# Kernel tuning notes

Measured on AMD Instinct MI355X. Metric: run time of the kernel, lower is better.

The kernel has to match this reference:

```python
import jax, jax.numpy as jnp
import numpy as np

EPS = 1e-12  # torch F.normalize eps

def _l2norm(t):
    # normalize over last axis (tokens N), matching F.normalize(dim=-1)
    n = jnp.sqrt(jnp.sum(t * t, axis=-1, keepdims=True))
    return t / jnp.maximum(n, EPS)

def setup_inputs() -> dict:
    key = jax.random.key(0)
    ks = jax.random.split(key, 4)
    B, N, C, H = 16, 3136, 768, 16
    x = jax.random.normal(ks[0], (B, N, C), dtype=jnp.float32)
    w_qkv = jax.random.normal(ks[1], (3 * C, C), dtype=jnp.float32) * (C ** -0.5)
    temperature = jnp.ones((H, 1, 1), dtype=jnp.float32)
    w_proj = jax.random.normal(ks[2], (C, C), dtype=jnp.float32) * (C ** -0.5)
    b_proj = jnp.zeros((C,), dtype=jnp.float32)
    return {"x": x, "w_qkv": w_qkv, "temperature": temperature,
            "w_proj": w_proj, "b_proj": b_proj}

def reference(x, w_qkv, temperature, w_proj, b_proj):
    B, N, C = x.shape
    H = temperature.shape[0]
    dh = C // H
    # qkv: [B,N,3C] -> [B,N,3,H,dh] -> [3,B,H,dh,N]
    qkv = (x @ w_qkv.T).reshape(B, N, 3, H, dh)
    qkv = jnp.transpose(qkv, (2, 0, 3, 4, 1))
    q, k, v = qkv[0], qkv[1], qkv[2]          # each [B,H,dh,N]
    q = _l2norm(q)
    k = _l2norm(k)
    # cross-covariance attention over channel axis: [B,H,dh,dh]
    attn = jnp.einsum('bhdn,bhen->bhde', q, k) * temperature
    attn = jax.nn.softmax(attn, axis=-1)
    out = jnp.einsum('bhde,bhen->bhdn', attn, v)  # [B,H,dh,N]
    out = jnp.transpose(out, (0, 3, 1, 2)).reshape(B, N, C)
    return out @ w_proj.T + b_proj
```

## Files before the change

kernel.cpp:

```cpp
#include <hip/hip_runtime.h>
#include <hip/hip_bf16.h>
#include <stdint.h>

using f32x4   = __attribute__((ext_vector_type(4))) float;
using half8   = __attribute__((ext_vector_type(8))) _Float16;
using half4   = __attribute__((ext_vector_type(4))) _Float16;
using float4v = __attribute__((ext_vector_type(4))) float;

typedef const __attribute__((address_space(1))) void gas_void;
typedef __attribute__((address_space(3))) void las_void;

__device__ __forceinline__ void gload_lds16(const void* gptr, void* lptr) {
  __builtin_amdgcn_global_load_lds((gas_void*)(uintptr_t)gptr,
                                   (las_void*)(uintptr_t)lptr, 16, 0, 0);
}

#define MFMA_F16(a, b, c) __builtin_amdgcn_mfma_f32_16x16x32_f16((a), (b), (c), 0, 0, 0)

__global__ void k_cvtw(const float* __restrict__ wqkv, const float* __restrict__ wproj,
                       _Float16* __restrict__ w16, _Float16* __restrict__ wp16,
                       _Float16* __restrict__ wvT) {
  const long N1 = 221184L, N2 = 73728L, N3 = 98304L;
  const long total = N1 + N2 + N3;
  for (long i = (long)blockIdx.x * blockDim.x + threadIdx.x; i < total;
       i += (long)gridDim.x * blockDim.x) {
    if (i < N1 + N2) {
      const float* src; _Float16* dst; long off;
      if (i < N1) { src = wqkv;  dst = w16;  off = i; }
      else        { src = wproj; dst = wp16; off = i - N1; }
      const float4v* p = (const float4v*)(src + off * 8);
      float4v a = p[0], b = p[1];
      half8 o;
      o[0] = (_Float16)a[0]; o[1] = (_Float16)a[1]; o[2] = (_Float16)a[2]; o[3] = (_Float16)a[3];
      o[4] = (_Float16)b[0]; o[5] = (_Float16)b[1]; o[6] = (_Float16)b[2]; o[7] = (_Float16)b[3];
      *(half8*)(dst + off * 8) = o;
    } else {
      const long u = i - N1 - N2;
      const int h = (int)(u / 6144);
      const int r = (int)(u % 6144);
      const int f = r >> 3, e0 = (r & 7) * 8;
      half8 o;
      if (e0 >= 48) {
#pragma unroll
        for (int j = 0; j < 8; ++j) o[j] = (_Float16)0.f;
      } else {
#pragma unroll
        for (int j = 0; j < 8; ++j)
          o[j] = (_Float16)wqkv[(long)(1536 + h * 48 + e0 + j) * 768 + f];
      }
      *(half8*)(wvT + ((long)(h * 768 + f) * 64 + e0)) = o;
    }
  }
}

__global__ __launch_bounds__(256)
void k_cvtx(const float* __restrict__ x, _Float16* __restrict__ x16,
            _Float16* __restrict__ xT) {
  __shared__ _Float16 lt[64 * 68];
  const int bid = blockIdx.x;
  const int b = bid / 588;
  const int rem = bid % 588;
  const int tt = rem / 12, ct = rem % 12;
  const long t0g = (long)b * 3136 + tt * 64;
  const int c0 = ct * 64;
  const int tid = threadIdx.x;
#pragma unroll
  for (int ch = 0; ch < 4; ++ch) {
    const int idx = tid + ch * 256;
    const int tr = idx >> 4, cg = (idx & 15) * 4;
    float4v v = *(const float4v*)&x[(t0g + tr) * 768 + c0 + cg];
    half4 hv;
    hv[0] = (_Float16)v[0]; hv[1] = (_Float16)v[1];
    hv[2] = (_Float16)v[2]; hv[3] = (_Float16)v[3];
    *(half4*)&x16[(t0g + tr) * 768 + c0 + cg] = hv;
    *(half4*)&lt[tr * 68 + cg] = hv;
  }
  __syncthreads();
  const int c = tid >> 2, tch = tid & 3;
  half8 o0, o1;
#pragma unroll
  for (int j = 0; j < 8; ++j) o0[j] = lt[(tch * 16 + j) * 68 + c];
#pragma unroll
  for (int j = 0; j < 8; ++j) o1[j] = lt[(tch * 16 + 8 + j) * 68 + c];
  _Float16* dst = xT + (long)b * 2408448 + (long)(c0 + c) * 3136 + tt * 64 + tch * 16;
  *(half8*)dst = o0;
  *(half8*)(dst + 8) = o1;
}

__global__ __launch_bounds__(256)
void k_gram(const _Float16* __restrict__ xT, _Float16* __restrict__ G) {
  __shared__ _Float16 lds[2][2][128 * 32];
  const int tid = threadIdx.x;
  const int wv = tid >> 6, lane = tid & 63;
  const int g = lane >> 4, cidx = lane & 15;
  const int wr = wv >> 1, wc = wv & 1;

  const int nwg = (int)gridDim.x;
  const int q = nwg >> 3, r = nwg & 7;
  const int xcd = (int)blockIdx.x & 7, bidx = (int)blockIdx.x >> 3;
  int wg = (xcd < r ? xcd * (q + 1) : r * (q + 1) + (xcd - r) * q) + bidx;
  const int b = wg / 21;
  int p = wg % 21;
  int mt = 0;
  while (p >= 6 - mt) { p -= 6 - mt; ++mt; }
  const int nt = mt + p;

  const _Float16* Ab = xT + (long)b * 2408448 + (long)mt * 128 * 3136;
  const _Float16* Bb = xT + (long)b * 2408448 + (long)nt * 128 * 3136;

  const int srow = lane >> 2;
  const int sgr  = (lane & 3) ^ ((lane >> 3) & 3);

  auto stage = [&](int buf, int kt) {
#pragma unroll
    for (int l = 0; l < 2; ++l) {
      const int rbase = wv * 32 + l * 16;
      const long koff = (long)kt * 32 + sgr * 8;
      gload_lds16(Ab + (long)(rbase + srow) * 3136 + koff, &lds[buf][0][rbase * 32]);
      gload_lds16(Bb + (long)(rbase + srow) * 3136 + koff, &lds[buf][1][rbase * 32]);
    }
  };
  const int gr = (g ^ ((cidx >> 1) & 3)) * 8;

  f32x4 acc[4][4] = {};
  stage(0, 0);
  __syncthreads();
  for (int kt = 0; kt < 98; ++kt) {
    const int cur = kt & 1;
    if (kt + 1 < 98) stage(cur ^ 1, kt + 1);
    half8 af[4], bf[4];
#pragma unroll
    for (int m = 0; m < 4; ++m)
      af[m] = *(const half8*)&lds[cur][0][(wr * 64 + m * 16 + cidx) * 32 + gr];
#pragma unroll
    for (int n = 0; n < 4; ++n)
      bf[n] = *(const half8*)&lds[cur][1][(wc * 64 + n * 16 + cidx) * 32 + gr];
#pragma unroll
    for (int m = 0; m < 4; ++m)
#pragma unroll
      for (int n = 0; n < 4; ++n)
        acc[m][n] = MFMA_F16(af[m], bf[n], acc[m][n]);
    __syncthreads();
  }
  _Float16* Gb = G + (long)b * 589824;
  const long m0 = (long)mt * 128, n0 = (long)nt * 128;
#pragma unroll
  for (int m = 0; m < 4; ++m)
#pragma unroll
    for (int rr = 0; rr < 4; ++rr) {
      const long row = m0 + wr * 64 + m * 16 + g * 4 + rr;
#pragma unroll
      for (int n = 0; n < 4; ++n)
        Gb[row * 768 + n0 + wc * 64 + n * 16 + cidx] = (_Float16)acc[m][n][rr];
    }
  if (mt != nt) {
#pragma unroll
    for (int m = 0; m < 4; ++m)
#pragma unroll
      for (int n = 0; n < 4; ++n) {
        half4 hv;
#pragma unroll
        for (int rr = 0; rr < 4; ++rr) hv[rr] = (_Float16)acc[m][n][rr];
        const long col  = n0 + wc * 64 + n * 16 + cidx;
        const long row0 = m0 + wr * 64 + m * 16 + g * 4;
        *(half4*)&Gb[col * 768 + row0] = hv;
      }
  }
}

template<bool OUT_F32>
__global__ __launch_bounds__(256)
void k_g128(const _Float16* __restrict__ A, const _Float16* __restrict__ B,
            void* __restrict__ Cv, const float* __restrict__ bias,
            int Mt, int Nt, long Areal, long Astr, long Bstr, long Cstr,
            long N, long K)
{
  __shared__ _Float16 lds[2][2][128 * 32];
  const int tid = threadIdx.x;
  const int wv = tid >> 6, lane = tid & 63;
  const int g = lane >> 4, cidx = lane & 15;
  const int wr = wv >> 1, wc = wv & 1;

  const int nwg = (int)gridDim.x;
  const int q = nwg >> 3, r = nwg & 7;
  const int xcd = (int)blockIdx.x & 7, bidx = (int)blockIdx.x >> 3;
  int wg = (xcd < r ? xcd * (q + 1) : r * (q + 1) + (xcd - r) * q) + bidx;
  const int tpb = Mt * Nt;
  const int b = wg / tpb;
  const int rem = wg % tpb;
  const int mt = rem % Mt, nt = rem / Mt;
  const long m0 = (long)mt * 128, n0 = (long)nt * 128;

  const _Float16* Ab = A + b * Astr + m0 * K;
  const _Float16* Bb = B + b * Bstr + n0 * K;
  const int nkt = (int)(K >> 5);

  const int srow = lane >> 2;
  const int sgr  = (lane & 3) ^ ((lane >> 3) & 3);

  auto stage = [&](int buf, int kt) {
#pragma unroll
    for (int l = 0; l < 2; ++l) {
      const int rbase = wv * 32 + l * 16;
      const long koff = (long)kt * 32 + sgr * 8;
      gload_lds16(Ab + (long)(rbase + srow) * K + koff, &lds[buf][0][rbase * 32]);
      gload_lds16(Bb + (long)(rbase + srow) * K + koff, &lds[buf][1][rbase * 32]);
    }
  };
  const int gr = (g ^ ((cidx >> 1) & 3)) * 8;

  f32x4 acc[4][4] = {};
  stage(0, 0);
  __syncthreads();
  for (int kt = 0; kt < nkt; ++kt) {
    const int cur = kt & 1;
    if (kt + 1 < nkt) stage(cur ^ 1, kt + 1);
    half8 af[4], bf[4];
#pragma unroll
    for (int m = 0; m < 4; ++m)
      af[m] = *(const half8*)&lds[cur][0][(wr * 64 + m * 16 + cidx) * 32 + gr];
#pragma unroll
    for (int n = 0; n < 4; ++n)
      bf[n] = *(const half8*)&lds[cur][1][(wc * 64 + n * 16 + cidx) * 32 + gr];
#pragma unroll
    for (int m = 0; m < 4; ++m)
#pragma unroll
      for (int n = 0; n < 4; ++n)
        acc[m][n] = MFMA_F16(af[m], bf[n], acc[m][n]);
    __syncthreads();
  }

  float bv[4] = {0.f, 0.f, 0.f, 0.f};
  if (bias) {
#pragma unroll
    for (int n = 0; n < 4; ++n) bv[n] = bias[n0 + wc * 64 + n * 16 + cidx];
  }
  if constexpr (OUT_F32) {
    float* C = (float*)Cv + b * Cstr;
#pragma unroll
    for (int m = 0; m < 4; ++m)
#pragma unroll
      for (int rr = 0; rr < 4; ++rr) {
        const long row = m0 + wr * 64 + m * 16 + g * 4 + rr;
        if (row < Areal) {
#pragma unroll
          for (int n = 0; n < 4; ++n)
            C[row * N + n0 + wc * 64 + n * 16 + cidx] = acc[m][n][rr] + bv[n];
        }
      }
  } else {
    _Float16* C = (_Float16*)Cv + b * Cstr;
#pragma unroll
    for (int m = 0; m < 4; ++m)
#pragma unroll
      for (int rr = 0; rr < 4; ++rr) {
        const long row = m0 + wr * 64 + m * 16 + g * 4 + rr;
        if (row < Areal) {
#pragma unroll
          for (int n = 0; n < 4; ++n)
            C[row * N + n0 + wc * 64 + n * 16 + cidx] = (_Float16)acc[m][n][rr];
        }
      }
  }
}

template<bool OUT_F32>
__global__ __launch_bounds__(512, 2)
void k_gemm8p(const _Float16* __restrict__ A, const _Float16* __restrict__ B,
              void* __restrict__ Cv, const float* __restrict__ bias,
              int Mt, int Nt, long Areal, long Astr, long Bstr, long Cstr,
              long N, long K)
{
  __shared__ _Float16 lds[65536];
  const int tid  = threadIdx.x;
  const int wv   = tid >> 6, lane = tid & 63;
  const int g    = lane >> 4, cidx = lane & 15;
  const int wr   = wv >> 2, wc = wv & 3;

  const int nwg = (int)gridDim.x;
  const int q = nwg >> 3, r = nwg & 7;
  const int xcd = (int)blockIdx.x & 7, bidx = (int)blockIdx.x >> 3;
  int wg = (xcd < r ? xcd * (q + 1) : r * (q + 1) + (xcd - r) * q) + bidx;

  const int tpb = Mt * Nt;
  const int b   = wg / tpb;
  const int rem = wg - b * tpb;
  const long mt = rem % Mt, nt = rem / Mt;
  const long m0 = mt * 256, n0 = nt * 256;

  const int NT = (int)(K >> 6);
  const int NI = NT >> 1;

  const _Float16* Ab = A + b * Astr + m0 * K;
  const _Float16* Bb = B + b * Bstr + n0 * K;

  const int srow = lane >> 2;
  const int sgr  = (lane & 3) ^ ((lane >> 3) & 3);

  auto stage = [&](int op, int buf, int kh, int t) {
    const _Float16* src = op ? Bb : Ab;
    const long koff = (long)t * 64 + kh * 32 + sgr * 8;
#pragma unroll
    for (int l = 0; l < 2; ++l) {
      const int chunk = l * 8 + wv;
      gload_lds16(src + (long)(chunk * 16 + srow) * K + koff,
                  &lds[buf * 32768 + op * 16384 + kh * 8192 + chunk * 512]);
    }
  };

  const int gr  = (g ^ ((cidx >> 1) & 3)) * 8;
  const int raA = (wr * 128 + cidx) * 32 + gr;
  const int raB = 16384 + (wc * 64 + cidx) * 32 + gr;

  f32x4 acc[8][4] = {};

  stage(0, 0, 0, 0); stage(1, 0, 0, 0);
  stage(0, 0, 1, 0); stage(1, 0, 1, 0);
  stage(0, 1, 0, 1); stage(1, 1, 0, 1);
  asm volatile("s_waitcnt vmcnt(4)" ::: "memory");
  __builtin_amdgcn_sched_barrier(0);
  __builtin_amdgcn_s_barrier();

  half8 afA[4], afB[4], bfA[4], bfB[4];
#pragma unroll
  for (int mm = 0; mm < 4; ++mm) afA[mm] = *(const half8*)&lds[raA + mm * 512];
#pragma unroll
  for (int nn = 0; nn < 4; ++nn) bfA[nn] = *(const half8*)&lds[raB + nn * 512];

#define XPH(CURA, CURB, MLO, NA, NBUF, NKS, NMLO, LOADB, NB, STAGE, BDRY)      \
  {                                                                            \
    STAGE;                                                                     \
    if (BDRY) {                                                                \
      asm volatile("s_waitcnt vmcnt(4)" ::: "memory");                         \
      __builtin_amdgcn_sched_barrier(0);                                       \
    }                                                                          \
    __builtin_amdgcn_s_barrier();                                              \
    _Pragma("unroll")                                                          \
    for (int mm = 0; mm < 4; ++mm)                                             \
      NA[mm] = *(const half8*)&lds[(NBUF)*32768 + (NKS)*8192 + raA + ((NMLO)+mm)*512]; \
    if (LOADB) {                                                               \
      _Pragma("unroll")                                                        \
      for (int nn = 0; nn < 4; ++nn)                                           \
        NB[nn] = *(const half8*)&lds[(NBUF)*32768 + (NKS)*8192 + raB + nn*512]; \
    }                                                                          \
    __builtin_amdgcn_sched_barrier(0);                                         \
    __builtin_amdgcn_s_setprio(1);                                             \
    _Pragma("unroll")                                                          \
    for (int mm = 0; mm < 4; ++mm)                                             \
      _Pragma("unroll")                                                        \
      for (int nn = 0; nn < 4; ++nn)                                           \
        acc[(MLO)+mm][nn] = MFMA_F16(CURA[mm], CURB[nn], acc[(MLO)+mm][nn]);   \
    __builtin_amdgcn_s_setprio(0);                                             \
    __builtin_amdgcn_s_barrier();                                              \
  }

  for (int it = 0; it < NI; ++it) {
    const int t1c = 2 * it + 1;
    int tn2 = 2 * it + 2; if (tn2 >= NT) tn2 -= NT;
    int tn3 = 2 * it + 3; if (tn3 >= NT) tn3 -= NT;
    XPH(afA, bfA, 0, afB, 0, 0, 4, 0, bfB, stage(0, 1, 1, t1c), false)
    XPH(afB, bfA, 4, afA, 0, 1, 0, 1, bfB, stage(1, 1, 1, t1c), false)
    XPH(afA, bfB, 0, afB, 0, 1, 4, 0, bfA, stage(0, 0, 0, tn2), false)
    XPH(afB, bfB, 4, afA, 1, 0, 0, 1, bfA, stage(1, 0, 0, tn2), true )
    XPH(afA, bfA, 0, afB, 1, 0, 4, 0, bfB, stage(0, 0, 1, tn2), false)
    XPH(afB, bfA, 4, afA, 1, 1, 0, 1, bfB, stage(1, 0, 1, tn2), false)
    XPH(afA, bfB, 0, afB, 1, 1, 4, 0, bfA, stage(0, 1, 0, tn3), false)
    XPH(afB, bfB, 4, afA, 0, 0, 0, 1, bfA, stage(1, 1, 0, tn3), true )
  }
#undef XPH

  float bv[4] = {0.f, 0.f, 0.f, 0.f};
  if (bias) {
#pragma unroll
    for (int n = 0; n < 4; ++n) bv[n] = bias[n0 + wc * 64 + n * 16 + cidx];
  }
  if constexpr (OUT_F32) {
    float* C = (float*)Cv + b * Cstr;
#pragma unroll
    for (int m = 0; m < 8; ++m)
#pragma unroll
      for (int rr = 0; rr < 4; ++rr) {
        const long row = m0 + wr * 128 + m * 16 + g * 4 + rr;
        if (row < Areal) {
#pragma unroll
          for (int n = 0; n < 4; ++n)
            C[row * N + (n0 + wc * 64 + n * 16 + cidx)] = acc[m][n][rr] + bv[n];
        }
      }
  } else {
    _Float16* C = (_Float16*)Cv + b * Cstr;
#pragma unroll
    for (int m = 0; m < 8; ++m)
#pragma unroll
      for (int rr = 0; rr < 4; ++rr) {
        const long row = m0 + wr * 128 + m * 16 + g * 4 + rr;
        if (row < Areal) {
#pragma unroll
          for (int n = 0; n < 4; ++n)
            C[row * N + (n0 + wc * 64 + n * 16 + cidx)] = (_Float16)acc[m][n][rr];
        }
      }
  }
}

__global__ __launch_bounds__(256)
void k_heads(const _Float16* __restrict__ QG, const _Float16* __restrict__ w16,
             const _Float16* __restrict__ wvT, const float* __restrict__ temperature,
             _Float16* __restrict__ weffT)
{
  const int b = blockIdx.x >> 4, h = blockIdx.x & 15;
  const int tid = threadIdx.x;
  const int w = tid >> 6, lane = tid & 63;
  const int g = lane >> 4, c = lane & 15;

  __shared__ float red[4][48 * 48];
  __shared__ float redss[4][2][48];
  __shared__ float inv[2][48];
  __shared__ _Float16 Pb[48 * 64];

  const _Float16* QGq = QG + (long)b * 1179648 + (long)(h * 48) * 768;
  const _Float16* QGk = QGq + 768L * 768;
  const _Float16* Wq  = w16 + (long)(h * 48) * 768;
  const _Float16* Wk  = w16 + (long)(768 + h * 48) * 768;

  f32x4 aS[3][3] = {};
  f32x4 aq[3] = {};
  f32x4 ak[3] = {};
  for (int ks = w * 6; ks < w * 6 + 6; ++ks) {
    const int k0 = ks * 32 + g * 8;
    half8 t1[3], t3[3], wqf[3], wkf[3];
#pragma unroll
    for (int m = 0; m < 3; ++m) {
      const long ro = (long)(m * 16 + c) * 768 + k0;
      t1[m]  = *(const half8*)(QGq + ro);
      t3[m]  = *(const half8*)(QGk + ro);
      wqf[m] = *(const half8*)(Wq + ro);
      wkf[m] = *(const half8*)(Wk + ro);
    }
#pragma unroll
    for (int m = 0; m < 3; ++m) {
      aq[m] = MFMA_F16(t1[m], wqf[m], aq[m]);
      ak[m] = MFMA_F16(t3[m], wkf[m], ak[m]);
#pragma unroll
      for (int n = 0; n < 3; ++n)
        aS[m][n] = MFMA_F16(t1[m], wkf[n], aS[m][n]);
    }
  }

#pragma unroll
  for (int m = 0; m < 3; ++m) {
#pragma unroll
    for (int n = 0; n < 3; ++n)
#pragma unroll
      for (int rr = 0; rr < 4; ++rr)
        red[w][(m * 16 + g * 4 + rr) * 48 + n * 16 + c] = aS[m][n][rr];
#pragma unroll
    for (int rr = 0; rr < 4; ++rr)
      if (c == g * 4 + rr) {
        redss[w][0][m * 16 + c] = aq[m][rr];
        redss[w][1][m * 16 + c] = ak[m][rr];
      }
  }
  __syncthreads();

  if (tid < 96) {
    const int is_k = tid / 48, d = tid % 48;
    const float s = redss[0][is_k][d] + redss[1][is_k][d] + redss[2][is_k][d] + redss[3][is_k][d];
    inv[is_k][d] = 1.0f / fmaxf(sqrtf(s), 1e-12f);
  }
  __syncthreads();

  if (tid < 48) {
    const int d = tid;
    const float iq = inv[0][d] * temperature[h];
    float rowv[48];
    float mx = -3.0e38f;
#pragma unroll
    for (int e = 0; e < 48; ++e) {
      const int idx = d * 48 + e;
      float t = (red[0][idx] + red[1][idx] + red[2][idx] + red[3][idx]) * iq * inv[1][e];
      rowv[e] = t;
      mx = fmaxf(mx, t);
    }
    float sum = 0.f;
#pragma unroll
    for (int e = 0; e < 48; ++e) {
      const float pv = __expf(rowv[e] - mx);
      rowv[e] = pv;
      sum += pv;
    }
    const float is = 1.0f / sum;
#pragma unroll
    for (int e = 0; e < 48; ++e)
      Pb[d * 64 + e] = (_Float16)(rowv[e] * is);
#pragma unroll
    for (int e = 48; e < 64; ++e)
      Pb[d * 64 + e] = (_Float16)0.f;
  }
  __syncthreads();

  half8 pf[3][2];
#pragma unroll
  for (int nf = 0; nf < 3; ++nf)
#pragma unroll
    for (int ks = 0; ks < 2; ++ks)
      pf[nf][ks] = *(const half8*)&Pb[(nf * 16 + c) * 64 + ks * 32 + g * 8];

  const _Float16* wvh = wvT + (long)h * 768 * 64;
  _Float16* wout = weffT + (long)b * 589824 + h * 48;

  for (int m = 0; m < 12; ++m) {
    const int f0 = w * 192 + m * 16;
    half8 va[2];
#pragma unroll
    for (int ks = 0; ks < 2; ++ks)
      va[ks] = *(const half8*)&wvh[(long)(f0 + c) * 64 + ks * 32 + g * 8];
    f32x4 a3[3] = {};
#pragma unroll
    for (int ks = 0; ks < 2; ++ks)
#pragma unroll
      for (int nf = 0; nf < 3; ++nf)
        a3[nf] = MFMA_F16(va[ks], pf[nf][ks], a3[nf]);
#pragma unroll
    for (int nf = 0; nf < 3; ++nf)
#pragma unroll
      for (int rr = 0; rr < 4; ++rr)
        wout[(long)(f0 + g * 4 + rr) * 768 + nf * 16 + c] = (_Float16)a3[nf][rr];
  }
}

extern "C" void kernel_launch(void* const* d_in, const int* in_sizes, int n_in,
                              void* d_out, int out_size, void* d_ws, size_t ws_size,
                              hipStream_t stream)
{
  (void)in_sizes; (void)n_in; (void)out_size; (void)ws_size;
  const float* x      = (const float*)d_in[0];
  const float* w_qkv  = (const float*)d_in[1];
  const float* temp   = (const float*)d_in[2];
  const float* w_proj = (const float*)d_in[3];
  const float* b_proj = (const float*)d_in[4];
  float* out = (float*)d_out;

  char* ws = (char*)d_ws;
  _Float16* x16   = (_Float16*)(ws);
  _Float16* xT    = (_Float16*)(ws + 77070336L);
  _Float16* G     = (_Float16*)(ws + 154140672L);
  _Float16* QG    = (_Float16*)(ws + 173015040L);
  _Float16* weffT = (_Float16*)(ws + 210763776L);
  _Float16* wfin  = (_Float16*)(ws + 229638144L);
  _Float16* w16   = (_Float16*)(ws + 248512512L);
  _Float16* wp16  = (_Float16*)(ws + 252051456L);
  _Float16* wvT   = (_Float16*)(ws + 253231104L);

  k_cvtw<<<768, 256, 0, stream>>>(w_qkv, w_proj, w16, wp16, wvT);
  k_cvtx<<<9408, 256, 0, stream>>>(x, x16, xT);
  k_gram<<<336, 256, 0, stream>>>(xT, G);
  k_gemm8p<false><<<288, 512, 0, stream>>>(w16, G, QG, nullptr,
                                           6, 3, 1536, 0, 589824, 1179648, 768, 768);
  k_heads<<<256, 256, 0, stream>>>(QG, w16, wvT, temp, weffT);
  k_g128<false><<<576, 256, 0, stream>>>(wp16, weffT, wfin, nullptr,
                                         6, 6, 768, 0, 589824, 589824, 768, 768);
  k_gemm8p<true><<<624, 512, 0, stream>>>(x16, wfin, out, b_proj,
                                          13, 3, 3136, 3136L * 768, 589824, 3136L * 768,
                                          768, 768);
}
```

Baseline: 338.9 us.

## Merge weight conversion into x conversion and widen gram kernel to 8 waves

Folds the weight fp32-to-fp16 conversion kernel into the x conversion launch as extra blocks, which removes one kernel launch and lets both run concurrently. The gram kernel moves to 512 threads (8 waves, 2x4 wave grid) with a K-tile of 64 instead of 32 and a new XOR swizzle, halving the number of main-loop iterations and barriers. Each wave now holds a 64x32 sub-tile, so its accumulator count is halved. LDS use doubles to 64 KB per block, which may lower occupancy.

```diff
diff --git a/kernel.cpp b/kernel.cpp
--- a/kernel.cpp
+++ b/kernel.cpp
@@ -17,47 +17,48 @@
 
 #define MFMA_F16(a, b, c) __builtin_amdgcn_mfma_f32_16x16x32_f16((a), (b), (c), 0, 0, 0)
 
-__global__ void k_cvtw(const float* __restrict__ wqkv, const float* __restrict__ wproj,
-                       _Float16* __restrict__ w16, _Float16* __restrict__ wp16,
-                       _Float16* __restrict__ wvT) {
-  const long N1 = 221184L, N2 = 73728L, N3 = 98304L;
-  const long total = N1 + N2 + N3;
-  for (long i = (long)blockIdx.x * blockDim.x + threadIdx.x; i < total;
-       i += (long)gridDim.x * blockDim.x) {
-    if (i < N1 + N2) {
-      const float* src; _Float16* dst; long off;
-      if (i < N1) { src = wqkv;  dst = w16;  off = i; }
-      else        { src = wproj; dst = wp16; off = i - N1; }
-      const float4v* p = (const float4v*)(src + off * 8);
-      float4v a = p[0], b = p[1];
-      half8 o;
-      o[0] = (_Float16)a[0]; o[1] = (_Float16)a[1]; o[2] = (_Float16)a[2]; o[3] = (_Float16)a[3];
-      o[4] = (_Float16)b[0]; o[5] = (_Float16)b[1]; o[6] = (_Float16)b[2]; o[7] = (_Float16)b[3];
-      *(half8*)(dst + off * 8) = o;
-    } else {
-      const long u = i - N1 - N2;
-      const int h = (int)(u / 6144);
-      const int r = (int)(u % 6144);
-      const int f = r >> 3, e0 = (r & 7) * 8;
-      half8 o;
-      if (e0 >= 48) {
-#pragma unroll
-        for (int j = 0; j < 8; ++j) o[j] = (_Float16)0.f;
-      } else {
-#pragma unroll
-        for (int j = 0; j < 8; ++j)
-          o[j] = (_Float16)wqkv[(long)(1536 + h * 48 + e0 + j) * 768 + f];
-      }
-      *(half8*)(wvT + ((long)(h * 768 + f) * 64 + e0)) = o;
-    }
-  }
-}
-
 __global__ __launch_bounds__(256)
 void k_cvtx(const float* __restrict__ x, _Float16* __restrict__ x16,
-            _Float16* __restrict__ xT) {
+            _Float16* __restrict__ xT,
+            const float* __restrict__ wqkv, const float* __restrict__ wproj,
+            _Float16* __restrict__ w16, _Float16* __restrict__ wp16,
+            _Float16* __restrict__ wvT) {
+  const int bid = blockIdx.x;
+  if (bid >= 9408) {
+    const long N1 = 221184L, N2 = 73728L, N3 = 98304L;
+    const long total = N1 + N2 + N3;
+    for (long i = (long)(bid - 9408) * blockDim.x + threadIdx.x; i < total;
+         i += 512L * blockDim.x) {
+      if (i < N1 + N2) {
+        const float* src; _Float16* dst; long off;
+        if (i < N1) { src = wqkv;  dst = w16;  off = i; }
+        else        { src = wproj; dst = wp16; off = i - N1; }
+        const float4v* p = (const float4v*)(src + off * 8);
+        float4v a = p[0], b = p[1];
+        half8 o;
+        o[0] = (_Float16)a[0]; o[1] = (_Float16)a[1]; o[2] = (_Float16)a[2]; o[3] = (_Float16)a[3];
+        o[4] = (_Float16)b[0]; o[5] = (_Float16)b[1]; o[6] = (_Float16)b[2]; o[7] = (_Float16)b[3];
+        *(half8*)(dst + off * 8) = o;
+      } else {
+        const long u = i - N1 - N2;
+        const int h = (int)(u / 6144);
+        const int r = (int)(u % 6144);
+        const int f = r >> 3, e0 = (r & 7) * 8;
+        half8 o;
+        if (e0 >= 48) {
+#pragma unroll
+          for (int j = 0; j < 8; ++j) o[j] = (_Float16)0.f;
+        } else {
+#pragma unroll
+          for (int j = 0; j < 8; ++j)
+            o[j] = (_Float16)wqkv[(long)(1536 + h * 48 + e0 + j) * 768 + f];
+        }
+        *(half8*)(wvT + ((long)(h * 768 + f) * 64 + e0)) = o;
+      }
+    }
+    return;
+  }
   __shared__ _Float16 lt[64 * 68];
-  const int bid = blockIdx.x;
   const int b = bid / 588;
   const int rem = bid % 588;
   const int tt = rem / 12, ct = rem % 12;
@@ -87,13 +88,13 @@
   *(half8*)(dst + 8) = o1;
 }
 
-__global__ __launch_bounds__(256)
+__global__ __launch_bounds__(512)
 void k_gram(const _Float16* __restrict__ xT, _Float16* __restrict__ G) {
-  __shared__ _Float16 lds[2][2][128 * 32];
+  __shared__ _Float16 lds[2][2][128 * 64];
   const int tid = threadIdx.x;
   const int wv = tid >> 6, lane = tid & 63;
   const int g = lane >> 4, cidx = lane & 15;
-  const int wr = wv >> 1, wc = wv & 1;
+  const int wr = wv >> 2, wc = wv & 3;
 
   const int nwg = (int)gridDim.x;
   const int q = nwg >> 3, r = nwg & 7;
@@ -108,38 +109,44 @@
   const _Float16* Ab = xT + (long)b * 2408448 + (long)mt * 128 * 3136;
   const _Float16* Bb = xT + (long)b * 2408448 + (long)nt * 128 * 3136;
 
-  const int srow = lane >> 2;
-  const int sgr  = (lane & 3) ^ ((lane >> 3) & 3);
+  const int srow8 = lane >> 3;
+  const int sgr8  = (lane & 7) ^ srow8;
 
   auto stage = [&](int buf, int kt) {
 #pragma unroll
     for (int l = 0; l < 2; ++l) {
-      const int rbase = wv * 32 + l * 16;
-      const long koff = (long)kt * 32 + sgr * 8;
-      gload_lds16(Ab + (long)(rbase + srow) * 3136 + koff, &lds[buf][0][rbase * 32]);
-      gload_lds16(Bb + (long)(rbase + srow) * 3136 + koff, &lds[buf][1][rbase * 32]);
+      const int chunk = l * 8 + wv;
+      const long grow = chunk * 8 + srow8;
+      const long koff = (long)kt * 64 + sgr8 * 8;
+      gload_lds16(Ab + grow * 3136 + koff, &lds[buf][0][chunk * 512]);
+      gload_lds16(Bb + grow * 3136 + koff, &lds[buf][1][chunk * 512]);
     }
   };
-  const int gr = (g ^ ((cidx >> 1) & 3)) * 8;
-
-  f32x4 acc[4][4] = {};
+
+  f32x4 acc[4][2] = {};
   stage(0, 0);
   __syncthreads();
-  for (int kt = 0; kt < 98; ++kt) {
+  for (int kt = 0; kt < 49; ++kt) {
     const int cur = kt & 1;
-    if (kt + 1 < 98) stage(cur ^ 1, kt + 1);
-    half8 af[4], bf[4];
-#pragma unroll
-    for (int m = 0; m < 4; ++m)
-      af[m] = *(const half8*)&lds[cur][0][(wr * 64 + m * 16 + cidx) * 32 + gr];
-#pragma unroll
-    for (int n = 0; n < 4; ++n)
-      bf[n] = *(const half8*)&lds[cur][1][(wc * 64 + n * 16 + cidx) * 32 + gr];
-#pragma unroll
-    for (int m = 0; m < 4; ++m)
-#pragma unroll
-      for (int n = 0; n < 4; ++n)
-        acc[m][n] = MFMA_F16(af[m], bf[n], acc[m][n]);
+    if (kt + 1 < 49) stage(cur ^ 1, kt + 1);
+    half8 af[4][2], bf[2][2];
+#pragma unroll
+    for (int ks = 0; ks < 2; ++ks) {
+      const int gran = (((ks << 2) + g) ^ (cidx & 7)) * 8;
+#pragma unroll
+      for (int m = 0; m < 4; ++m)
+        af[m][ks] = *(const half8*)&lds[cur][0][(wr * 64 + m * 16 + cidx) * 64 + gran];
+#pragma unroll
+      for (int n = 0; n < 2; ++n)
+        bf[n][ks] = *(const half8*)&lds[cur][1][(wc * 32 + n * 16 + cidx) * 64 + gran];
+    }
+#pragma unroll
+    for (int ks = 0; ks < 2; ++ks)
+#pragma unroll
+      for (int m = 0; m < 4; ++m)
+#pragma unroll
+        for (int n = 0; n < 2; ++n)
+          acc[m][n] = MFMA_F16(af[m][ks], bf[n][ks], acc[m][n]);
     __syncthreads();
   }
   _Float16* Gb = G + (long)b * 589824;
@@ -150,18 +157,18 @@
     for (int rr = 0; rr < 4; ++rr) {
       const long row = m0 + wr * 64 + m * 16 + g * 4 + rr;
 #pragma unroll
-      for (int n = 0; n < 4; ++n)
-        Gb[row * 768 + n0 + wc * 64 + n * 16 + cidx] = (_Float16)acc[m][n][rr];
+      for (int n = 0; n < 2; ++n)
+        Gb[row * 768 + n0 + wc * 32 + n * 16 + cidx] = (_Float16)acc[m][n][rr];
     }
   if (mt != nt) {
 #pragma unroll
     for (int m = 0; m < 4; ++m)
 #pragma unroll
-      for (int n = 0; n < 4; ++n) {
+      for (int n = 0; n < 2; ++n) {
         half4 hv;
 #pragma unroll
         for (int rr = 0; rr < 4; ++rr) hv[rr] = (_Float16)acc[m][n][rr];
-        const long col  = n0 + wc * 64 + n * 16 + cidx;
+        const long col  = n0 + wc * 32 + n * 16 + cidx;
         const long row0 = m0 + wr * 64 + m * 16 + g * 4;
         *(half4*)&Gb[col * 768 + row0] = hv;
       }
@@ -552,9 +559,8 @@
   _Float16* wp16  = (_Float16*)(ws + 252051456L);
   _Float16* wvT   = (_Float16*)(ws + 253231104L);
 
-  k_cvtw<<<768, 256, 0, stream>>>(w_qkv, w_proj, w16, wp16, wvT);
-  k_cvtx<<<9408, 256, 0, stream>>>(x, x16, xT);
-  k_gram<<<336, 256, 0, stream>>>(xT, G);
+  k_cvtx<<<9920, 256, 0, stream>>>(x, x16, xT, w_qkv, w_proj, w16, wp16, wvT);
+  k_gram<<<336, 512, 0, stream>>>(xT, G);
   k_gemm8p<false><<<288, 512, 0, stream>>>(w16, G, QG, nullptr,
                                            6, 3, 1536, 0, 589824, 1179648, 768, 768);
   k_heads<<<256, 256, 0, stream>>>(QG, w16, wvT, temp, weffT);
```

New measurement: 319.7 us. -5.7%, faster.
